# Performance work log

Hardware: AMD Instinct MI355X
Metric: run time of the kernel (lower is better)

Reference implementation:

```python
import jax, jax.numpy as jnp
import numpy as np

B, S, D = 2, 2048, 2048
H, KVH, HD = 32, 8, 64
GROUPS = H // KVH  # 4
NEG = -1e9


def setup_inputs() -> dict:
    key = jax.random.key(0)
    ks = jax.random.split(key, 5)
    x = jax.random.normal(ks[0], (B, S, D), dtype=jnp.float32)
    # causal additive mask [1,1,S,S]
    causal = jnp.triu(jnp.full((S, S), NEG, dtype=jnp.float32), k=1)[None, None]
    Wq = jax.random.normal(ks[1], (D, D), dtype=jnp.float32) * (D ** -0.5)
    Wk = jax.random.normal(ks[2], (KVH * HD, D), dtype=jnp.float32) * (D ** -0.5)
    Wv = jax.random.normal(ks[3], (KVH * HD, D), dtype=jnp.float32) * (D ** -0.5)
    Wo = jax.random.normal(ks[4], (D, D), dtype=jnp.float32) * (D ** -0.5)
    return {"x": x, "attention_mask": causal, "Wq": Wq, "Wk": Wk, "Wv": Wv, "Wo": Wo}


def reference(x, attention_mask, Wq, Wk, Wv, Wo):
    b, s, _ = x.shape
    # projections (nn.Linear: y = x @ W.T)
    q = (x @ Wq.T).reshape(b, s, H, HD).transpose(0, 2, 1, 3)      # [b,H,s,hd]
    k = (x @ Wk.T).reshape(b, s, KVH, HD).transpose(0, 2, 1, 3)    # [b,KVH,s,hd]
    v = (x @ Wv.T).reshape(b, s, KVH, HD).transpose(0, 2, 1, 3)
    new_kv_cache = (k, v)
    # repeat_interleave over head dim for GQA
    k = jnp.repeat(k, GROUPS, axis=1)  # [b,H,s,hd]
    v = jnp.repeat(v, GROUPS, axis=1)
    scale = 1.0 / jnp.sqrt(jnp.float32(HD))
    scores = jnp.einsum('bhqd,bhkd->bhqk', q, k) * scale
    scores = scores + attention_mask
    attn = jax.nn.softmax(scores.astype(jnp.float32), axis=-1).astype(q.dtype)
    out = jnp.einsum('bhqk,bhkd->bhqd', attn, v)  # [b,H,s,hd]
    out = out.transpose(0, 2, 1, 3).reshape(b, s, H * HD)
    output = out @ Wo.T
    return (output, new_kv_cache[0], new_kv_cache[1])
```

## Files before the change

### kernel.cpp

```cpp
#include <hip/hip_runtime.h>
#include <hip/hip_bf16.h>
#include <stdint.h>

#define B_ 2
#define S_ 2048
#define D_ 2048
#define H_ 32
#define KVH_ 8
#define HD_ 64

typedef __bf16 bf16x8 __attribute__((ext_vector_type(8)));
typedef float f32x4 __attribute__((ext_vector_type(4)));

#define MFMA16(a, b, c) __builtin_amdgcn_mfma_f32_16x16x32_bf16((a), (b), (c), 0, 0, 0)

typedef __attribute__((address_space(1))) void gvoid_t;
typedef __attribute__((address_space(3))) void lvoid_t;

__device__ __forceinline__ void async_ld16(__hip_bfloat16* lds, const __hip_bfloat16* g) {
  __builtin_amdgcn_global_load_lds((gvoid_t*)(void*)(g), (lvoid_t*)(lds), 16, 0, 0);
}

__device__ __forceinline__ unsigned short f2bu(float f) {
  __hip_bfloat16 h = __float2bfloat16(f);
  return *reinterpret_cast<unsigned short*>(&h);
}

__global__ void cast_bf16_kernel(const float* __restrict__ in,
                                 unsigned short* __restrict__ out, int n4) {
  int i = blockIdx.x * blockDim.x + threadIdx.x;
  if (i >= n4) return;
  float4 v = reinterpret_cast<const float4*>(in)[i];
  ushort4 o;
  o.x = f2bu(v.x); o.y = f2bu(v.y); o.z = f2bu(v.z); o.w = f2bu(v.w);
  reinterpret_cast<ushort4*>(out)[i] = o;
}

template <int MODE>
__global__ __launch_bounds__(256, 2)
void gemm_bt(const __hip_bfloat16* __restrict__ A,
             const __hip_bfloat16* __restrict__ W,
             float* __restrict__ Cf, __hip_bfloat16* __restrict__ Cb,
             float* __restrict__ Cf2, __hip_bfloat16* __restrict__ Cb2,
             __hip_bfloat16* __restrict__ Cb3,
             int M, int N, int K) {
  __shared__ __align__(16) __hip_bfloat16 sA[128 * 32];
  __shared__ __align__(16) __hip_bfloat16 sB[128 * 32];
  const int tid = threadIdx.x;
  const int lane = tid & 63;
  const int wv = tid >> 6;
  const int l15 = lane & 15, l4 = lane >> 4;
  const int bm = blockIdx.x * 128, bn = blockIdx.y * 128;
  const int wm = (wv >> 1) * 64, wn = (wv & 1) * 64;

  const int ci0 = tid, ci1 = tid + 256;
  const __hip_bfloat16* gA0 = A + (size_t)(bm + (ci0 >> 2)) * K + (ci0 & 3) * 8;
  const __hip_bfloat16* gA1 = A + (size_t)(bm + (ci1 >> 2)) * K + (ci1 & 3) * 8;
  const __hip_bfloat16* gB0 = W + (size_t)(bn + (ci0 >> 2)) * K + (ci0 & 3) * 8;
  const __hip_bfloat16* gB1 = W + (size_t)(bn + (ci1 >> 2)) * K + (ci1 & 3) * 8;
  __hip_bfloat16* lA0 = &sA[ci0 * 8];
  __hip_bfloat16* lA1 = &sA[ci1 * 8];
  __hip_bfloat16* lB0 = &sB[ci0 * 8];
  __hip_bfloat16* lB1 = &sB[ci1 * 8];

  f32x4 acc[4][4];
#pragma unroll
  for (int i = 0; i < 4; ++i) {
#pragma unroll
    for (int j = 0; j < 4; ++j) acc[i][j] = f32x4{0.f, 0.f, 0.f, 0.f};
  }

  for (int k0 = 0; k0 < K; k0 += 32) {
    async_ld16(lA0, gA0 + k0);
    async_ld16(lA1, gA1 + k0);
    async_ld16(lB0, gB0 + k0);
    async_ld16(lB1, gB1 + k0);
    __syncthreads();
    bf16x8 af[4], bfr[4];
#pragma unroll
    for (int i = 0; i < 4; ++i)
      af[i] = *reinterpret_cast<const bf16x8*>(&sA[(wm + i * 16 + l15) * 32 + l4 * 8]);
#pragma unroll
    for (int j = 0; j < 4; ++j)
      bfr[j] = *reinterpret_cast<const bf16x8*>(&sB[(wn + j * 16 + l15) * 32 + l4 * 8]);
#pragma unroll
    for (int i = 0; i < 4; ++i) {
#pragma unroll
      for (int j = 0; j < 4; ++j) acc[i][j] = MFMA16(af[i], bfr[j], acc[i][j]);
    }
    __syncthreads();
  }

#pragma unroll
  for (int i = 0; i < 4; ++i) {
#pragma unroll
    for (int j = 0; j < 4; ++j) {
      const int col = bn + wn + j * 16 + l15;
#pragma unroll
      for (int r = 0; r < 4; ++r) {
        const int row = bm + wm + i * 16 + l4 * 4 + r;
        const float v = acc[i][j][r];
        if (MODE == 1) {
          Cf[(size_t)row * N + col] = v;
        } else {
          if (bn < 2048) {
            Cb[(size_t)row * 2048 + col] = __float2bfloat16(v);
          } else {
            const int bb = row >> 11, s = row & 2047;
            const int kv = col - 2048;
            if (kv < 512) {
              const int g = kv >> 6, hd = kv & 63;
              const size_t idx = ((size_t)(bb * KVH_ + g) * S_ + s) * HD_ + hd;
              Cf[idx] = v;
              Cb2[idx] = __float2bfloat16(v);
            } else {
              const int vv = kv - 512;
              const int g = vv >> 6, hd = vv & 63;
              const size_t idx = ((size_t)(bb * KVH_ + g) * S_ + s) * HD_ + hd;
              Cf2[idx] = v;
              Cb3[((size_t)(bb * KVH_ + g) * HD_ + hd) * S_ + s] = __float2bfloat16(v);
            }
          }
        }
      }
    }
  }
}

__global__ __launch_bounds__(512, 4)
void attn_fused(const __hip_bfloat16* __restrict__ Qb,
                const __hip_bfloat16* __restrict__ Kb,
                const __hip_bfloat16* __restrict__ Vtb,
                __hip_bfloat16* __restrict__ AOb) {
  __shared__ __align__(16) __hip_bfloat16 sK[2][64 * 64];
  __shared__ __align__(16) __hip_bfloat16 sV[2][64 * 64];
  __shared__ __align__(16) __hip_bfloat16 sP[8 * 32 * 64];

  const int tid = threadIdx.x;
  const int lane = tid & 63;
  const int wv = tid >> 6;
  const int l15 = lane & 15, l4 = lane >> 4;
  const int qa = blockIdx.x;
  const int qb = 15 - qa;
  const int isB = wv >> 2;
  const int wq = wv & 3;
  const int qt = isB ? qb : qa;
  const int h = blockIdx.y;
  const int b = blockIdx.z;
  const int g = h >> 2;

  bf16x8 qf[2][2];
  {
    const __hip_bfloat16* Qp =
        Qb + ((size_t)(b * S_ + qt * 128 + wq * 32)) * D_ + h * HD_;
#pragma unroll
    for (int i = 0; i < 2; ++i) {
#pragma unroll
      for (int c = 0; c < 2; ++c) {
        qf[i][c] = *reinterpret_cast<const bf16x8*>(
            Qp + (size_t)(i * 16 + l15) * D_ + c * 32 + l4 * 8);
      }
    }
  }

  f32x4 oacc[2][4];
  f32x4 lacc[2];
#pragma unroll
  for (int i = 0; i < 2; ++i) {
    lacc[i] = f32x4{0.f, 0.f, 0.f, 0.f};
#pragma unroll
    for (int j = 0; j < 4; ++j) oacc[i][j] = f32x4{0.f, 0.f, 0.f, 0.f};
  }

  bf16x8 vone;
#pragma unroll
  for (int j = 0; j < 8; ++j) vone[j] = (__bf16)1.0f;

  const __hip_bfloat16* Kp = Kb + (size_t)(b * KVH_ + g) * S_ * HD_;
  const __hip_bfloat16* Vp = Vtb + (size_t)(b * KVH_ + g) * HD_ * S_;
  __hip_bfloat16* sPw = sP + wv * (32 * 64);
  const float CE = 0.125f * 1.4426950408889634f;
  const float MSUB = 8.0f;

  const int r0 = tid >> 3, c0 = (tid & 7) ^ (r0 & 7);
  const __hip_bfloat16* gk = Kp + (size_t)r0 * HD_ + c0 * 8;
  const __hip_bfloat16* gv = Vp + (size_t)r0 * S_ + c0 * 8;

  auto stage = [&](int buf) {
    async_ld16(&sK[buf][tid * 8], gk);
    async_ld16(&sV[buf][tid * 8], gv);
    gk += 64 * HD_;
    gv += 64;
  };

  auto pack = [&](f32x4 (&sc)[2][4], int koff) {
    if (koff >= 0) {
#pragma unroll
      for (int i = 0; i < 2; ++i) {
#pragma unroll
        for (int jn = 0; jn < 4; ++jn) {
          const int kp = koff + jn * 16 + l15;
#pragma unroll
          for (int r = 0; r < 4; ++r) {
            const int qp = wq * 32 + i * 16 + l4 * 4 + r;
            if (kp > qp) sc[i][jn][r] = -3.0e38f;
          }
        }
      }
    }
#pragma unroll
    for (int i = 0; i < 2; ++i) {
#pragma unroll
      for (int jj = 0; jj < 4; ++jj) {
#pragma unroll
        for (int r = 0; r < 4; ++r) {
          const float p = exp2f(fmaf(sc[i][jj][r], CE, -MSUB));
          sPw[(i * 16 + l4 * 4 + r) * 64 + ((jj ^ l4) * 16 + l15)] =
              __float2bfloat16(p);
        }
      }
    }
  };

  const int nsteps = 2 * qb + 2;
  const int kmax = isB ? nsteps : (2 * qa + 2);
  stage(0);
  for (int ki = 0; ki < nsteps; ++ki) {
    const int cur = ki & 1;
    __syncthreads();
    if (ki + 1 < nsteps) stage(cur ^ 1);
    if (ki < kmax) {
      const int ko = ((ki >> 1) == qt) ? (ki & 1) * 64 : -1;

      f32x4 sc[2][4];
#pragma unroll
      for (int jn = 0; jn < 4; ++jn) {
        const int row = jn * 16 + l15;
        const bf16x8 k0 = *reinterpret_cast<const bf16x8*>(
            &sK[cur][(row * 8 + (l4 ^ (row & 7))) * 8]);
        const bf16x8 k1 = *reinterpret_cast<const bf16x8*>(
            &sK[cur][(row * 8 + ((4 + l4) ^ (row & 7))) * 8]);
#pragma unroll
        for (int i = 0; i < 2; ++i) {
          f32x4 t = f32x4{0.f, 0.f, 0.f, 0.f};
          t = MFMA16(qf[i][0], k0, t);
          t = MFMA16(qf[i][1], k1, t);
          sc[i][jn] = t;
        }
      }

      pack(sc, ko);

      const int gr = (l15 >> 2) & 3;
#pragma unroll
      for (int kc = 0; kc < 2; ++kc) {
        bf16x8 vf[4];
#pragma unroll
        for (int jn = 0; jn < 4; ++jn) {
          const int row = jn * 16 + l15;
          vf[jn] = *reinterpret_cast<const bf16x8*>(
              &sV[cur][(row * 8 + ((kc * 4 + l4) ^ (row & 7))) * 8]);
        }
        const int pcol = (((kc * 2 + (l4 >> 1)) ^ gr) * 16 + (l4 & 1) * 8);
#pragma unroll
        for (int i = 0; i < 2; ++i) {
          const bf16x8 pf = *reinterpret_cast<const bf16x8*>(
              &sPw[(i * 16 + l15) * 64 + pcol]);
#pragma unroll
          for (int jn = 0; jn < 4; ++jn) oacc[i][jn] = MFMA16(pf, vf[jn], oacc[i][jn]);
          lacc[i] = MFMA16(pf, vone, lacc[i]);
        }
      }
    }
  }

#pragma unroll
  for (int i = 0; i < 2; ++i) {
    float inv[4];
#pragma unroll
    for (int r = 0; r < 4; ++r) inv[r] = 1.0f / lacc[i][r];
#pragma unroll
    for (int jn = 0; jn < 4; ++jn) {
#pragma unroll
      for (int r = 0; r < 4; ++r) {
        const int qp = qt * 128 + wq * 32 + i * 16 + l4 * 4 + r;
        AOb[(size_t)(b * S_ + qp) * D_ + h * HD_ + jn * 16 + l15] =
            __float2bfloat16(oacc[i][jn][r] * inv[r]);
      }
    }
  }
}

extern "C" void kernel_launch(void* const* d_in, const int* in_sizes, int n_in,
                              void* d_out, int out_size, void* d_ws, size_t ws_size,
                              hipStream_t stream) {
  (void)in_sizes; (void)n_in; (void)out_size; (void)ws_size;
  const float* x = (const float*)d_in[0];
  const float* Wq = (const float*)d_in[2];
  const float* Wk = (const float*)d_in[3];
  const float* Wv = (const float*)d_in[4];
  const float* Wo = (const float*)d_in[5];

  float* outO = (float*)d_out;
  float* outK = outO + (size_t)B_ * S_ * D_;
  float* outV = outK + (size_t)B_ * KVH_ * S_ * HD_;

  char* p = (char*)d_ws;
  __hip_bfloat16* xb    = (__hip_bfloat16*)p; p += (size_t)B_ * S_ * D_ * 2;
  __hip_bfloat16* Wqkvb = (__hip_bfloat16*)p; p += (size_t)3072 * D_ * 2;
  __hip_bfloat16* Wob   = (__hip_bfloat16*)p; p += (size_t)D_ * D_ * 2;
  __hip_bfloat16* Qbf   = (__hip_bfloat16*)p; p += (size_t)B_ * S_ * D_ * 2;
  __hip_bfloat16* Kbf   = (__hip_bfloat16*)p; p += (size_t)B_ * KVH_ * S_ * HD_ * 2;
  __hip_bfloat16* Vtb   = (__hip_bfloat16*)p; p += (size_t)B_ * KVH_ * S_ * HD_ * 2;
  __hip_bfloat16* AOb   = (__hip_bfloat16*)p; p += (size_t)B_ * S_ * D_ * 2;

  auto cast = [&](const float* src, __hip_bfloat16* dst, size_t n) {
    const int n4 = (int)(n / 4);
    cast_bf16_kernel<<<dim3((n4 + 255) / 256), dim3(256), 0, stream>>>(
        src, (unsigned short*)dst, n4);
  };
  cast(x, xb, (size_t)B_ * S_ * D_);
  cast(Wq, Wqkvb, (size_t)D_ * D_);
  cast(Wk, Wqkvb + (size_t)2048 * D_, (size_t)KVH_ * HD_ * D_);
  cast(Wv, Wqkvb + (size_t)2560 * D_, (size_t)KVH_ * HD_ * D_);
  cast(Wo, Wob, (size_t)D_ * D_);

  gemm_bt<4><<<dim3(32, 24), dim3(256), 0, stream>>>(
      xb, Wqkvb, outK, Qbf, outV, Kbf, Vtb, 4096, 3072, 2048);
  attn_fused<<<dim3(8, 32, 2), dim3(512), 0, stream>>>(Qbf, Kbf, Vtb, AOb);
  gemm_bt<1><<<dim3(32, 16), dim3(256), 0, stream>>>(
      AOb, Wob, outO, nullptr, nullptr, nullptr, nullptr, 4096, 2048, 2048);
}
```

Before: 327.5 us.

## Rewrite bf16 GEMMs with larger tiles, double-buffered LDS and swizzle

Replaces the 128x128 single-buffered GEMM with a templated 256xBN tile kernel using 512 threads, K-step 64 split into two 32-wide planes, and double-buffered LDS so global-to-LDS loads for future tiles overlap MFMA work. Adds an XOR swizzle on LDS columns to reduce bank conflicts and uses s_setprio around MFMA blocks. The QKV GEMM uses a 256x256 tile and the output GEMM 256x128. The cost is more LDS and registers per block, fewer blocks in the grid (192 and 256), and hand-placed waitcnt counts that must match the number of loads in flight.

```diff
diff --git a/kernel.cpp b/kernel.cpp
--- a/kernel.cpp
+++ b/kernel.cpp
@@ -36,70 +36,130 @@
   reinterpret_cast<ushort4*>(out)[i] = o;
 }
 
-template <int MODE>
-__global__ __launch_bounds__(256, 2)
-void gemm_bt(const __hip_bfloat16* __restrict__ A,
-             const __hip_bfloat16* __restrict__ W,
-             float* __restrict__ Cf, __hip_bfloat16* __restrict__ Cb,
-             float* __restrict__ Cf2, __hip_bfloat16* __restrict__ Cb2,
-             __hip_bfloat16* __restrict__ Cb3,
-             int M, int N, int K) {
-  __shared__ __align__(16) __hip_bfloat16 sA[128 * 32];
-  __shared__ __align__(16) __hip_bfloat16 sB[128 * 32];
+template <int MODE, int BN, int WAVES_M, int WAVES_N>
+__global__ __launch_bounds__(512, 2)
+void gemm_bt2(const __hip_bfloat16* __restrict__ A,
+              const __hip_bfloat16* __restrict__ W,
+              float* __restrict__ Cf, __hip_bfloat16* __restrict__ Cb,
+              float* __restrict__ Cf2, __hip_bfloat16* __restrict__ Cb2,
+              __hip_bfloat16* __restrict__ Cb3,
+              int M, int N, int K) {
+  constexpr int BM = 256;
+  constexpr int WM = BM / WAVES_M;
+  constexpr int WN = BN / WAVES_N;
+  constexpr int MR = WM / 16;
+  constexpr int NR = WN / 16;
+  constexpr int A_PLANE = BM * 32;
+  constexpr int B_PLANE = BN * 32;
+  constexpr int BUF_E = 2 * (A_PLANE + B_PLANE);
+  constexpr int ACH = A_PLANE / (512 * 8);
+  constexpr int BCH = B_PLANE / (512 * 8);
+  constexpr int LPT = 2 * (ACH + BCH);
+
+  __shared__ __align__(16) __hip_bfloat16 sAB[2 * BUF_E];
+
   const int tid = threadIdx.x;
   const int lane = tid & 63;
   const int wv = tid >> 6;
   const int l15 = lane & 15, l4 = lane >> 4;
-  const int bm = blockIdx.x * 128, bn = blockIdx.y * 128;
-  const int wm = (wv >> 1) * 64, wn = (wv & 1) * 64;
-
-  const int ci0 = tid, ci1 = tid + 256;
-  const __hip_bfloat16* gA0 = A + (size_t)(bm + (ci0 >> 2)) * K + (ci0 & 3) * 8;
-  const __hip_bfloat16* gA1 = A + (size_t)(bm + (ci1 >> 2)) * K + (ci1 & 3) * 8;
-  const __hip_bfloat16* gB0 = W + (size_t)(bn + (ci0 >> 2)) * K + (ci0 & 3) * 8;
-  const __hip_bfloat16* gB1 = W + (size_t)(bn + (ci1 >> 2)) * K + (ci1 & 3) * 8;
-  __hip_bfloat16* lA0 = &sA[ci0 * 8];
-  __hip_bfloat16* lA1 = &sA[ci1 * 8];
-  __hip_bfloat16* lB0 = &sB[ci0 * 8];
-  __hip_bfloat16* lB1 = &sB[ci1 * 8];
-
-  f32x4 acc[4][4];
-#pragma unroll
-  for (int i = 0; i < 4; ++i) {
-#pragma unroll
-    for (int j = 0; j < 4; ++j) acc[i][j] = f32x4{0.f, 0.f, 0.f, 0.f};
-  }
-
-  for (int k0 = 0; k0 < K; k0 += 32) {
-    async_ld16(lA0, gA0 + k0);
-    async_ld16(lA1, gA1 + k0);
-    async_ld16(lB0, gB0 + k0);
-    async_ld16(lB1, gB1 + k0);
-    __syncthreads();
-    bf16x8 af[4], bfr[4];
-#pragma unroll
-    for (int i = 0; i < 4; ++i)
-      af[i] = *reinterpret_cast<const bf16x8*>(&sA[(wm + i * 16 + l15) * 32 + l4 * 8]);
-#pragma unroll
-    for (int j = 0; j < 4; ++j)
-      bfr[j] = *reinterpret_cast<const bf16x8*>(&sB[(wn + j * 16 + l15) * 32 + l4 * 8]);
-#pragma unroll
-    for (int i = 0; i < 4; ++i) {
-#pragma unroll
-      for (int j = 0; j < 4; ++j) acc[i][j] = MFMA16(af[i], bfr[j], acc[i][j]);
-    }
-    __syncthreads();
-  }
-
-#pragma unroll
-  for (int i = 0; i < 4; ++i) {
-#pragma unroll
-    for (int j = 0; j < 4; ++j) {
-      const int col = bn + wn + j * 16 + l15;
+  const int bm = blockIdx.x * BM, bn = blockIdx.y * BN;
+  const int wmo = (wv / WAVES_N) * WM;
+  const int wno = (wv % WAVES_N) * WN;
+
+  const __hip_bfloat16* gA[ACH];
+  const __hip_bfloat16* gB[BCH];
+#pragma unroll
+  for (int i = 0; i < ACH; ++i) {
+    const int ch = tid + i * 512;
+    const int row = ch >> 2, pc = ch & 3;
+    const int c = pc ^ ((row >> 1) & 3);
+    gA[i] = A + (size_t)(bm + row) * K + c * 8;
+  }
+#pragma unroll
+  for (int i = 0; i < BCH; ++i) {
+    const int ch = tid + i * 512;
+    const int row = ch >> 2, pc = ch & 3;
+    const int c = pc ^ ((row >> 1) & 3);
+    gB[i] = W + (size_t)(bn + row) * K + c * 8;
+  }
+
+  int offA[MR], offB[NR];
+#pragma unroll
+  for (int mi = 0; mi < MR; ++mi) {
+    const int row = wmo + mi * 16 + l15;
+    offA[mi] = row * 32 + ((l4 ^ ((row >> 1) & 3)) * 8);
+  }
+#pragma unroll
+  for (int nj = 0; nj < NR; ++nj) {
+    const int row = wno + nj * 16 + l15;
+    offB[nj] = row * 32 + ((l4 ^ ((row >> 1) & 3)) * 8);
+  }
+
+  f32x4 acc[MR][NR];
+#pragma unroll
+  for (int i = 0; i < MR; ++i)
+#pragma unroll
+    for (int j = 0; j < NR; ++j) acc[i][j] = f32x4{0.f, 0.f, 0.f, 0.f};
+
+  auto stagekk = [&](int buf, int kk, int kbase) {
+    __hip_bfloat16* dA = &sAB[buf * BUF_E + kk * A_PLANE];
+    __hip_bfloat16* dB = &sAB[buf * BUF_E + 2 * A_PLANE + kk * B_PLANE];
+#pragma unroll
+    for (int i = 0; i < ACH; ++i)
+      async_ld16(dA + (tid + i * 512) * 8, gA[i] + kbase);
+#pragma unroll
+    for (int i = 0; i < BCH; ++i)
+      async_ld16(dB + (tid + i * 512) * 8, gB[i] + kbase);
+  };
+
+  const int NT = K >> 6;
+  stagekk(0, 0, 0);  stagekk(0, 1, 32);
+  stagekk(1, 0, 64); stagekk(1, 1, 96);
+  if constexpr (LPT == 8) asm volatile("s_waitcnt vmcnt(8)" ::: "memory");
+  else                    asm volatile("s_waitcnt vmcnt(6)" ::: "memory");
+  __builtin_amdgcn_s_barrier();
+
+  int cur = 0;
+  for (int t = 0; t < NT; ++t) {
+    const int tpre = (t + 2 < NT) ? (t + 2) : (NT - 1);
+#pragma unroll
+    for (int kk = 0; kk < 2; ++kk) {
+      const __hip_bfloat16* pa = &sAB[cur * BUF_E + kk * A_PLANE];
+      const __hip_bfloat16* pb = &sAB[cur * BUF_E + 2 * A_PLANE + kk * B_PLANE];
+      bf16x8 af[MR], bfv[NR];
+#pragma unroll
+      for (int mi = 0; mi < MR; ++mi)
+        af[mi] = *reinterpret_cast<const bf16x8*>(&pa[offA[mi]]);
+#pragma unroll
+      for (int nj = 0; nj < NR; ++nj)
+        bfv[nj] = *reinterpret_cast<const bf16x8*>(&pb[offB[nj]]);
+      __builtin_amdgcn_s_setprio(1);
+#pragma unroll
+      for (int mi = 0; mi < MR; ++mi)
+#pragma unroll
+        for (int nj = 0; nj < NR; ++nj)
+          acc[mi][nj] = MFMA16(af[mi], bfv[nj], acc[mi][nj]);
+      __builtin_amdgcn_s_setprio(0);
+      asm volatile("s_waitcnt lgkmcnt(0)" ::: "memory");
+      __builtin_amdgcn_sched_barrier(0);
+      __builtin_amdgcn_s_barrier();
+      stagekk(cur, kk, tpre * 64 + kk * 32);
+    }
+    if constexpr (LPT == 8) asm volatile("s_waitcnt vmcnt(8)" ::: "memory");
+    else                    asm volatile("s_waitcnt vmcnt(6)" ::: "memory");
+    __builtin_amdgcn_s_barrier();
+    cur ^= 1;
+  }
+
+#pragma unroll
+  for (int mi = 0; mi < MR; ++mi) {
+#pragma unroll
+    for (int nj = 0; nj < NR; ++nj) {
+      const int col = bn + wno + nj * 16 + l15;
 #pragma unroll
       for (int r = 0; r < 4; ++r) {
-        const int row = bm + wm + i * 16 + l4 * 4 + r;
-        const float v = acc[i][j][r];
+        const int row = bm + wmo + mi * 16 + l4 * 4 + r;
+        const float v = acc[mi][nj][r];
         if (MODE == 1) {
           Cf[(size_t)row * N + col] = v;
         } else {
@@ -325,9 +385,9 @@
   cast(Wv, Wqkvb + (size_t)2560 * D_, (size_t)KVH_ * HD_ * D_);
   cast(Wo, Wob, (size_t)D_ * D_);
 
-  gemm_bt<4><<<dim3(32, 24), dim3(256), 0, stream>>>(
+  gemm_bt2<4, 256, 2, 4><<<dim3(16, 12), dim3(512), 0, stream>>>(
       xb, Wqkvb, outK, Qbf, outV, Kbf, Vtb, 4096, 3072, 2048);
   attn_fused<<<dim3(8, 32, 2), dim3(512), 0, stream>>>(Qbf, Kbf, Vtb, AOb);
-  gemm_bt<1><<<dim3(32, 16), dim3(256), 0, stream>>>(
+  gemm_bt2<1, 128, 4, 2><<<dim3(16, 16), dim3(512), 0, stream>>>(
       AOb, Wob, outO, nullptr, nullptr, nullptr, nullptr, 4096, 2048, 2048);
 }
```

Measured after the change: 337.7 us. 1.03x slower.
